# Kernel optimization log

Measured on AMD Instinct MI355X. Metric: run time of the kernel, lower is better.

Reference implementation:

```python
import jax, jax.numpy as jnp
import numpy as np

B, H, K, L, V = 4096, 1024, 10, 64, 80  # batch, hidden, mixtures, char_len, vocab

def setup_inputs() -> dict:
    key = jax.random.key(0)
    k1, k2, k3, k4 = jax.random.split(key, 4)
    return {
        "x": jax.random.normal(k1, (B, H), dtype=jnp.float32),
        "chars": jax.random.normal(k2, (B, L, V), dtype=jnp.float32),
        "W": jax.random.normal(k3, (H, 3 * K), dtype=jnp.float32) * 0.02,
        "b": jax.random.normal(k4, (3 * K,), dtype=jnp.float32) * 0.02,
    }

def reference(x, chars, W, b):
    # Linear: [B, 3K]
    out = x @ W + b
    alpha_raw, beta_raw, kappa_raw = jnp.split(out, 3, axis=1)  # each [B, K]
    alpha = jnp.exp(alpha_raw)[:, :, None]            # [B, K, 1]
    beta = jnp.exp(beta_raw)[:, :, None]              # [B, K, 1]
    # kappa_prev is zero on first call -> kappa = exp(kappa_raw)
    kappa = jnp.exp(kappa_raw)[:, :, None]            # [B, K, 1]
    u = jnp.arange(L, dtype=jnp.float32)[None, None, :]  # [1, 1, L]
    phi = jnp.sum(alpha * jnp.exp(-beta * (kappa - u) ** 2), axis=1)  # [B, L]
    window = jnp.einsum('bl,blv->bv', phi, chars)     # [B, V]
    return window
```

## Files before the change

kernel.cpp:

```cpp
#include <hip/hip_runtime.h>
#include <math.h>

constexpr int Bn = 4096;
constexpr int Hn = 1024;
constexpr int Kn = 10;
constexpr int Ln = 64;
constexpr int Vn = 80;
constexpr int NJ = 3 * Kn;
constexpr int R  = 4;
constexpr int NT = 256;

__global__ __launch_bounds__(NT) void window_kernel(
    const float* __restrict__ x,
    const float* __restrict__ chars,
    const float* __restrict__ W,
    const float* __restrict__ bias,
    float* __restrict__ out)
{
    __shared__ float  xs[R * Hn];
    __shared__ float  part[R * 256];
    __shared__ float  abk[R * NJ];
    __shared__ float  phi_s[R * Ln];
    __shared__ float4 cpart[R * 12 * 20];

    const int t    = threadIdx.x;
    const int row0 = blockIdx.x * R;

    const float4* x4  = (const float4*)x;
    float4*       xs4 = (float4*)xs;
#pragma unroll
    for (int r = 0; r < R; ++r)
        xs4[r * (Hn / 4) + t] = x4[(size_t)(row0 + r) * (Hn / 4) + t];
    __syncthreads();

    const int j = t & 31;
    const int g = t >> 5;
    float acc0 = 0.f, acc1 = 0.f, acc2 = 0.f, acc3 = 0.f;
    if (j < NJ) {
        const float* Wp = W + j;
        const int h0 = g * 128;
#pragma unroll 4
        for (int ii = 0; ii < 128; ii += 4) {
            const int h  = h0 + ii;
            const int h4 = h >> 2;
            float4 xa = xs4[0 * (Hn / 4) + h4];
            float4 xb = xs4[1 * (Hn / 4) + h4];
            float4 xc = xs4[2 * (Hn / 4) + h4];
            float4 xd = xs4[3 * (Hn / 4) + h4];
            float w0 = Wp[(h + 0) * NJ];
            float w1 = Wp[(h + 1) * NJ];
            float w2 = Wp[(h + 2) * NJ];
            float w3 = Wp[(h + 3) * NJ];
            acc0 += w0 * xa.x + w1 * xa.y + w2 * xa.z + w3 * xa.w;
            acc1 += w0 * xb.x + w1 * xb.y + w2 * xb.z + w3 * xb.w;
            acc2 += w0 * xc.x + w1 * xc.y + w2 * xc.z + w3 * xc.w;
            acc3 += w0 * xd.x + w1 * xd.y + w2 * xd.z + w3 * xd.w;
        }
    }
    part[0 * 256 + g * 32 + j] = acc0;
    part[1 * 256 + g * 32 + j] = acc1;
    part[2 * 256 + g * 32 + j] = acc2;
    part[3 * 256 + g * 32 + j] = acc3;
    __syncthreads();

    if (t < R * NJ) {
        const int r = t / NJ, jj = t % NJ;
        float s = bias[jj];
#pragma unroll
        for (int gg = 0; gg < 8; ++gg) s += part[r * 256 + gg * 32 + jj];
        abk[r * NJ + jj] = __expf(s);
    }
    __syncthreads();

    {
        const int r = t >> 6, l = t & 63;
        const float lf = (float)l;
        const float* ab = abk + r * NJ;
        float ph = 0.f;
#pragma unroll
        for (int k = 0; k < Kn; ++k) {
            float a  = ab[k];
            float bt = ab[Kn + k];
            float kp = ab[2 * Kn + k];
            float d  = kp - lf;
            ph += a * __expf(-bt * d * d);
        }
        phi_s[r * Ln + l] = ph;
    }
    __syncthreads();

    const float4* c4 = (const float4*)chars;
    if (t < 240) {
        const int v4  = t % 20;
        const int g12 = t / 20;
        float4 s0 = make_float4(0.f, 0.f, 0.f, 0.f);
        float4 s1 = s0, s2 = s0, s3 = s0;
        for (int l = g12; l < Ln; l += 12) {
            const int off = l * 20 + v4;
            float4 cA = c4[(size_t)(row0 + 0) * 1280 + off];
            float4 cB = c4[(size_t)(row0 + 1) * 1280 + off];
            float4 cC = c4[(size_t)(row0 + 2) * 1280 + off];
            float4 cD = c4[(size_t)(row0 + 3) * 1280 + off];
            float p0 = phi_s[0 * Ln + l];
            float p1 = phi_s[1 * Ln + l];
            float p2 = phi_s[2 * Ln + l];
            float p3 = phi_s[3 * Ln + l];
            s0.x += p0 * cA.x; s0.y += p0 * cA.y; s0.z += p0 * cA.z; s0.w += p0 * cA.w;
            s1.x += p1 * cB.x; s1.y += p1 * cB.y; s1.z += p1 * cB.z; s1.w += p1 * cB.w;
            s2.x += p2 * cC.x; s2.y += p2 * cC.y; s2.z += p2 * cC.z; s2.w += p2 * cC.w;
            s3.x += p3 * cD.x; s3.y += p3 * cD.y; s3.z += p3 * cD.z; s3.w += p3 * cD.w;
        }
        cpart[(0 * 12 + g12) * 20 + v4] = s0;
        cpart[(1 * 12 + g12) * 20 + v4] = s1;
        cpart[(2 * 12 + g12) * 20 + v4] = s2;
        cpart[(3 * 12 + g12) * 20 + v4] = s3;
    }
    __syncthreads();

    if (t < 80) {
        const int r  = t / 20;
        const int vv = t % 20;
        float4 s = make_float4(0.f, 0.f, 0.f, 0.f);
#pragma unroll
        for (int gg = 0; gg < 12; ++gg) {
            float4 p = cpart[(r * 12 + gg) * 20 + vv];
            s.x += p.x; s.y += p.y; s.z += p.z; s.w += p.w;
        }
        ((float4*)out)[(size_t)(row0 + r) * 20 + vv] = s;
    }
}

extern "C" void kernel_launch(void* const* d_in, const int* in_sizes, int n_in,
                              void* d_out, int out_size, void* d_ws, size_t ws_size,
                              hipStream_t stream) {
    const float* x     = (const float*)d_in[0];
    const float* chars = (const float*)d_in[1];
    const float* W     = (const float*)d_in[2];
    const float* bias  = (const float*)d_in[3];
    float* out = (float*)d_out;

    window_kernel<<<Bn / R, NT, 0, stream>>>(x, chars, W, bias, out);
}
```

Baseline: 141.7 us.

## Split fused kernel into phi kernel and lighter-weight einsum kernel via workspace

Splits the single fused kernel into two. The first computes the linear projection and phi and writes phi to the workspace buffer. The second streams chars for 2 rows per block with small shared memory, so more blocks can be resident while the bandwidth-heavy einsum runs. The fused kernel stays as a fallback when no workspace is available. This adds a second launch and a global round-trip for phi.

```diff
diff --git a/kernel.cpp b/kernel.cpp
--- a/kernel.cpp
+++ b/kernel.cpp
@@ -9,19 +9,17 @@
 constexpr int NJ = 3 * Kn;
 constexpr int R  = 4;
 constexpr int NT = 256;
-
-__global__ __launch_bounds__(NT) void window_kernel(
+constexpr int RW = 2;
+
+__global__ __launch_bounds__(NT) void phi_kernel(
     const float* __restrict__ x,
-    const float* __restrict__ chars,
     const float* __restrict__ W,
     const float* __restrict__ bias,
-    float* __restrict__ out)
+    float* __restrict__ phi)
 {
-    __shared__ float  xs[R * Hn];
-    __shared__ float  part[R * 256];
-    __shared__ float  abk[R * NJ];
-    __shared__ float  phi_s[R * Ln];
-    __shared__ float4 cpart[R * 12 * 20];
+    __shared__ float xs[R * Hn];
+    __shared__ float part[R * 256];
+    __shared__ float abk[R * NJ];
 
     const int t    = threadIdx.x;
     const int row0 = blockIdx.x * R;
@@ -85,6 +83,133 @@
             float d  = kp - lf;
             ph += a * __expf(-bt * d * d);
         }
+        phi[(size_t)(row0 + r) * Ln + l] = ph;
+    }
+}
+
+__global__ __launch_bounds__(NT) void einsum_kernel(
+    const float* __restrict__ phi,
+    const float* __restrict__ chars,
+    float* __restrict__ out)
+{
+    __shared__ float  phi_s[RW * Ln];
+    __shared__ float4 cpart[RW * 12 * 20];
+
+    const int t    = threadIdx.x;
+    const int row0 = blockIdx.x * RW;
+
+    if (t < RW * Ln)
+        phi_s[t] = phi[(size_t)row0 * Ln + t];
+    __syncthreads();
+
+    const float4* c4 = (const float4*)chars;
+    if (t < 240) {
+        const int v4 = t % 20;
+        const int g  = t / 20;
+        float4 s0 = make_float4(0.f, 0.f, 0.f, 0.f);
+        float4 s1 = s0;
+        for (int l = g; l < Ln; l += 12) {
+            const int off = l * 20 + v4;
+            float4 cA = c4[(size_t)(row0 + 0) * 1280 + off];
+            float4 cB = c4[(size_t)(row0 + 1) * 1280 + off];
+            float p0 = phi_s[l];
+            float p1 = phi_s[Ln + l];
+            s0.x += p0 * cA.x; s0.y += p0 * cA.y; s0.z += p0 * cA.z; s0.w += p0 * cA.w;
+            s1.x += p1 * cB.x; s1.y += p1 * cB.y; s1.z += p1 * cB.z; s1.w += p1 * cB.w;
+        }
+        cpart[(0 * 12 + g) * 20 + v4] = s0;
+        cpart[(1 * 12 + g) * 20 + v4] = s1;
+    }
+    __syncthreads();
+
+    if (t < RW * 20) {
+        const int r  = t / 20;
+        const int vv = t % 20;
+        float4 s = make_float4(0.f, 0.f, 0.f, 0.f);
+#pragma unroll
+        for (int gg = 0; gg < 12; ++gg) {
+            float4 p = cpart[(r * 12 + gg) * 20 + vv];
+            s.x += p.x; s.y += p.y; s.z += p.z; s.w += p.w;
+        }
+        ((float4*)out)[(size_t)(row0 + r) * 20 + vv] = s;
+    }
+}
+
+__global__ __launch_bounds__(NT) void window_kernel(
+    const float* __restrict__ x,
+    const float* __restrict__ chars,
+    const float* __restrict__ W,
+    const float* __restrict__ bias,
+    float* __restrict__ out)
+{
+    __shared__ float  xs[R * Hn];
+    __shared__ float  part[R * 256];
+    __shared__ float  abk[R * NJ];
+    __shared__ float  phi_s[R * Ln];
+    __shared__ float4 cpart[R * 12 * 20];
+
+    const int t    = threadIdx.x;
+    const int row0 = blockIdx.x * R;
+
+    const float4* x4  = (const float4*)x;
+    float4*       xs4 = (float4*)xs;
+#pragma unroll
+    for (int r = 0; r < R; ++r)
+        xs4[r * (Hn / 4) + t] = x4[(size_t)(row0 + r) * (Hn / 4) + t];
+    __syncthreads();
+
+    const int j = t & 31;
+    const int g = t >> 5;
+    float acc0 = 0.f, acc1 = 0.f, acc2 = 0.f, acc3 = 0.f;
+    if (j < NJ) {
+        const float* Wp = W + j;
+        const int h0 = g * 128;
+#pragma unroll 4
+        for (int ii = 0; ii < 128; ii += 4) {
+            const int h  = h0 + ii;
+            const int h4 = h >> 2;
+            float4 xa = xs4[0 * (Hn / 4) + h4];
+            float4 xb = xs4[1 * (Hn / 4) + h4];
+            float4 xc = xs4[2 * (Hn / 4) + h4];
+            float4 xd = xs4[3 * (Hn / 4) + h4];
+            float w0 = Wp[(h + 0) * NJ];
+            float w1 = Wp[(h + 1) * NJ];
+            float w2 = Wp[(h + 2) * NJ];
+            float w3 = Wp[(h + 3) * NJ];
+            acc0 += w0 * xa.x + w1 * xa.y + w2 * xa.z + w3 * xa.w;
+            acc1 += w0 * xb.x + w1 * xb.y + w2 * xb.z + w3 * xb.w;
+            acc2 += w0 * xc.x + w1 * xc.y + w2 * xc.z + w3 * xc.w;
+            acc3 += w0 * xd.x + w1 * xd.y + w2 * xd.z + w3 * xd.w;
+        }
+    }
+    part[0 * 256 + g * 32 + j] = acc0;
+    part[1 * 256 + g * 32 + j] = acc1;
+    part[2 * 256 + g * 32 + j] = acc2;
+    part[3 * 256 + g * 32 + j] = acc3;
+    __syncthreads();
+
+    if (t < R * NJ) {
+        const int r = t / NJ, jj = t % NJ;
+        float s = bias[jj];
+#pragma unroll
+        for (int gg = 0; gg < 8; ++gg) s += part[r * 256 + gg * 32 + jj];
+        abk[r * NJ + jj] = __expf(s);
+    }
+    __syncthreads();
+
+    {
+        const int r = t >> 6, l = t & 63;
+        const float lf = (float)l;
+        const float* ab = abk + r * NJ;
+        float ph = 0.f;
+#pragma unroll
+        for (int k = 0; k < Kn; ++k) {
+            float a  = ab[k];
+            float bt = ab[Kn + k];
+            float kp = ab[2 * Kn + k];
+            float d  = kp - lf;
+            ph += a * __expf(-bt * d * d);
+        }
         phi_s[r * Ln + l] = ph;
     }
     __syncthreads();
@@ -139,5 +264,12 @@
     const float* bias  = (const float*)d_in[3];
     float* out = (float*)d_out;
 
-    window_kernel<<<Bn / R, NT, 0, stream>>>(x, chars, W, bias, out);
-}
+    const size_t phi_bytes = (size_t)Bn * Ln * sizeof(float);
+    if (d_ws != nullptr && ws_size >= phi_bytes) {
+        float* phi = (float*)d_ws;
+        phi_kernel<<<Bn / R, NT, 0, stream>>>(x, W, bias, phi);
+        einsum_kernel<<<Bn / RW, NT, 0, stream>>>(phi, chars, out);
+    } else {
+        window_kernel<<<Bn / R, NT, 0, stream>>>(x, chars, W, bias, out);
+    }
+}
```

After: 148.7 us. 1.05x slower.

## Prefetch chars into LDS asynchronously and halve rows per block

Applied to the files above, without the earlier changes.

Issues asynchronous global-to-LDS loads of each block's chars tile at kernel start, so the memory-bound chars stream overlaps with the linear layer and phi computation. Rows per block drop from four to two, doubling the grid for more parallelism, and the sync points become raw barriers. The cost is higher LDS use, which limits occupancy, and W is reread twice as often. There is some risk of wait-count ordering issues with the async loads.

```diff
diff --git a/kernel.cpp b/kernel.cpp
--- a/kernel.cpp
+++ b/kernel.cpp
@@ -1,5 +1,6 @@
 #include <hip/hip_runtime.h>
 #include <math.h>
+#include <stdint.h>
 
 constexpr int Bn = 4096;
 constexpr int Hn = 1024;
@@ -7,35 +8,56 @@
 constexpr int Ln = 64;
 constexpr int Vn = 80;
 constexpr int NJ = 3 * Kn;
-constexpr int R  = 4;
+constexpr int R  = 2;
 constexpr int NT = 256;
 
-__global__ __launch_bounds__(NT) void window_kernel(
+typedef const __attribute__((address_space(1))) uint32_t glb_u32;
+typedef __attribute__((address_space(3))) uint32_t lds_u32;
+__device__ __forceinline__ void gload_lds16(const void* g, void* l) {
+    __builtin_amdgcn_global_load_lds((glb_u32*)g, (lds_u32*)l, 16, 0, 0);
+}
+
+__global__ __launch_bounds__(NT) void window_fused(
     const float* __restrict__ x,
     const float* __restrict__ chars,
     const float* __restrict__ W,
     const float* __restrict__ bias,
     float* __restrict__ out)
 {
-    __shared__ float  xs[R * Hn];
-    __shared__ float  part[R * 256];
+    __shared__ float4 cs4[R * Ln * Vn / 4];
+    __shared__ float4 xs4[R * Hn / 4];
+    __shared__ float  red[R * 256];
     __shared__ float  abk[R * NJ];
     __shared__ float  phi_s[R * Ln];
-    __shared__ float4 cpart[R * 12 * 20];
 
     const int t    = threadIdx.x;
+    const int lane = t & 63;
+    const int w    = t >> 6;
     const int row0 = blockIdx.x * R;
 
-    const float4* x4  = (const float4*)x;
-    float4*       xs4 = (float4*)xs;
+    const float4* xg4 = (const float4*)(x + (size_t)row0 * Hn);
+    float4 xa = xg4[t];
+    float4 xb = xg4[NT + t];
+    float bias_v = 0.f;
+    if (t < R * NJ) bias_v = bias[t % NJ];
+    xs4[t]      = xa;
+    xs4[NT + t] = xb;
+
+    const char* cg = (const char*)(chars + (size_t)row0 * Ln * Vn);
+    char*       cl = (char*)cs4;
 #pragma unroll
-    for (int r = 0; r < R; ++r)
-        xs4[r * (Hn / 4) + t] = x4[(size_t)(row0 + r) * (Hn / 4) + t];
-    __syncthreads();
+    for (int i = 0; i < 10; ++i) {
+        const int off = (w * 10 + i) * 1024;
+        gload_lds16(cg + off + lane * 16, cl + off);
+    }
+
+    asm volatile("s_waitcnt lgkmcnt(0)" ::: "memory");
+    __builtin_amdgcn_s_barrier();
+    __builtin_amdgcn_sched_barrier(0);
 
     const int j = t & 31;
     const int g = t >> 5;
-    float acc0 = 0.f, acc1 = 0.f, acc2 = 0.f, acc3 = 0.f;
+    float acc0 = 0.f, acc1 = 0.f;
     if (j < NJ) {
         const float* Wp = W + j;
         const int h0 = g * 128;
@@ -43,36 +65,34 @@
         for (int ii = 0; ii < 128; ii += 4) {
             const int h  = h0 + ii;
             const int h4 = h >> 2;
-            float4 xa = xs4[0 * (Hn / 4) + h4];
-            float4 xb = xs4[1 * (Hn / 4) + h4];
-            float4 xc = xs4[2 * (Hn / 4) + h4];
-            float4 xd = xs4[3 * (Hn / 4) + h4];
+            float4 va = xs4[h4];
+            float4 vb = xs4[(Hn / 4) + h4];
             float w0 = Wp[(h + 0) * NJ];
             float w1 = Wp[(h + 1) * NJ];
             float w2 = Wp[(h + 2) * NJ];
             float w3 = Wp[(h + 3) * NJ];
-            acc0 += w0 * xa.x + w1 * xa.y + w2 * xa.z + w3 * xa.w;
-            acc1 += w0 * xb.x + w1 * xb.y + w2 * xb.z + w3 * xb.w;
-            acc2 += w0 * xc.x + w1 * xc.y + w2 * xc.z + w3 * xc.w;
-            acc3 += w0 * xd.x + w1 * xd.y + w2 * xd.z + w3 * xd.w;
+            acc0 += w0 * va.x + w1 * va.y + w2 * va.z + w3 * va.w;
+            acc1 += w0 * vb.x + w1 * vb.y + w2 * vb.z + w3 * vb.w;
         }
     }
-    part[0 * 256 + g * 32 + j] = acc0;
-    part[1 * 256 + g * 32 + j] = acc1;
-    part[2 * 256 + g * 32 + j] = acc2;
-    part[3 * 256 + g * 32 + j] = acc3;
-    __syncthreads();
+    red[0 * 256 + g * 32 + j] = acc0;
+    red[1 * 256 + g * 32 + j] = acc1;
+    asm volatile("s_waitcnt lgkmcnt(0)" ::: "memory");
+    __builtin_amdgcn_s_barrier();
+    __builtin_amdgcn_sched_barrier(0);
 
     if (t < R * NJ) {
         const int r = t / NJ, jj = t % NJ;
-        float s = bias[jj];
+        float s = bias_v;
 #pragma unroll
-        for (int gg = 0; gg < 8; ++gg) s += part[r * 256 + gg * 32 + jj];
+        for (int gg = 0; gg < 8; ++gg) s += red[r * 256 + gg * 32 + jj];
         abk[r * NJ + jj] = __expf(s);
     }
-    __syncthreads();
+    asm volatile("s_waitcnt lgkmcnt(0)" ::: "memory");
+    __builtin_amdgcn_s_barrier();
+    __builtin_amdgcn_sched_barrier(0);
 
-    {
+    if (t < R * Ln) {
         const int r = t >> 6, l = t & 63;
         const float lf = (float)l;
         const float* ab = abk + r * NJ;
@@ -87,37 +107,29 @@
         }
         phi_s[r * Ln + l] = ph;
     }
+
     __syncthreads();
 
-    const float4* c4 = (const float4*)chars;
+    float4* cpart = (float4*)xs4;
     if (t < 240) {
         const int v4  = t % 20;
         const int g12 = t / 20;
         float4 s0 = make_float4(0.f, 0.f, 0.f, 0.f);
-        float4 s1 = s0, s2 = s0, s3 = s0;
+        float4 s1 = s0;
         for (int l = g12; l < Ln; l += 12) {
-            const int off = l * 20 + v4;
-            float4 cA = c4[(size_t)(row0 + 0) * 1280 + off];
-            float4 cB = c4[(size_t)(row0 + 1) * 1280 + off];
-            float4 cC = c4[(size_t)(row0 + 2) * 1280 + off];
-            float4 cD = c4[(size_t)(row0 + 3) * 1280 + off];
-            float p0 = phi_s[0 * Ln + l];
-            float p1 = phi_s[1 * Ln + l];
-            float p2 = phi_s[2 * Ln + l];
-            float p3 = phi_s[3 * Ln + l];
+            float4 cA = cs4[l * 20 + v4];
+            float4 cB = cs4[1280 + l * 20 + v4];
+            float p0 = phi_s[l];
+            float p1 = phi_s[Ln + l];
             s0.x += p0 * cA.x; s0.y += p0 * cA.y; s0.z += p0 * cA.z; s0.w += p0 * cA.w;
             s1.x += p1 * cB.x; s1.y += p1 * cB.y; s1.z += p1 * cB.z; s1.w += p1 * cB.w;
-            s2.x += p2 * cC.x; s2.y += p2 * cC.y; s2.z += p2 * cC.z; s2.w += p2 * cC.w;
-            s3.x += p3 * cD.x; s3.y += p3 * cD.y; s3.z += p3 * cD.z; s3.w += p3 * cD.w;
         }
         cpart[(0 * 12 + g12) * 20 + v4] = s0;
         cpart[(1 * 12 + g12) * 20 + v4] = s1;
-        cpart[(2 * 12 + g12) * 20 + v4] = s2;
-        cpart[(3 * 12 + g12) * 20 + v4] = s3;
     }
     __syncthreads();
 
-    if (t < 80) {
+    if (t < R * 20) {
         const int r  = t / 20;
         const int vv = t % 20;
         float4 s = make_float4(0.f, 0.f, 0.f, 0.f);
@@ -139,5 +151,5 @@
     const float* bias  = (const float*)d_in[3];
     float* out = (float*)d_out;
 
-    window_kernel<<<Bn / R, NT, 0, stream>>>(x, chars, W, bias, out);
+    window_fused<<<Bn / R, NT, 0, stream>>>(x, chars, W, bias, out);
 }
```

Result: slower. 148.5 us (+4.8%).

## Map one wavefront per row for window reduction and reduce via shuffles

Applied to the files above, without the earlier changes.

The chars-weighted reduction is remapped so each 64-lane wavefront handles one batch row. Lanes split into three l-strided groups of 20 float4 columns, and the partials are combined with wave shuffles instead of a shared-memory cpart buffer and an extra barrier. This removes the last __syncthreads and the serial 12-way shared reduction, and shrinks shared memory. Launch bounds now request 7 blocks per CU for occupancy. Lanes 60-63 do redundant loads, and each lane performs more serial iterations (up to 22).

```diff
diff --git a/kernel.cpp b/kernel.cpp
--- a/kernel.cpp
+++ b/kernel.cpp
@@ -10,27 +10,25 @@
 constexpr int R  = 4;
 constexpr int NT = 256;
 
-__global__ __launch_bounds__(NT) void window_kernel(
+__global__ __launch_bounds__(NT, 7) void window_fused(
     const float* __restrict__ x,
     const float* __restrict__ chars,
     const float* __restrict__ W,
     const float* __restrict__ bias,
     float* __restrict__ out)
 {
-    __shared__ float  xs[R * Hn];
+    __shared__ float4 xs4[R * Hn / 4];
     __shared__ float  part[R * 256];
     __shared__ float  abk[R * NJ];
     __shared__ float  phi_s[R * Ln];
-    __shared__ float4 cpart[R * 12 * 20];
 
     const int t    = threadIdx.x;
     const int row0 = blockIdx.x * R;
 
-    const float4* x4  = (const float4*)x;
-    float4*       xs4 = (float4*)xs;
+    const float4* xg4 = (const float4*)x + (size_t)row0 * (Hn / 4);
 #pragma unroll
     for (int r = 0; r < R; ++r)
-        xs4[r * (Hn / 4) + t] = x4[(size_t)(row0 + r) * (Hn / 4) + t];
+        xs4[r * (Hn / 4) + t] = xg4[r * (Hn / 4) + t];
     __syncthreads();
 
     const int j = t & 31;
@@ -89,45 +87,34 @@
     }
     __syncthreads();
 
-    const float4* c4 = (const float4*)chars;
-    if (t < 240) {
-        const int v4  = t % 20;
-        const int g12 = t / 20;
-        float4 s0 = make_float4(0.f, 0.f, 0.f, 0.f);
-        float4 s1 = s0, s2 = s0, s3 = s0;
-        for (int l = g12; l < Ln; l += 12) {
-            const int off = l * 20 + v4;
-            float4 cA = c4[(size_t)(row0 + 0) * 1280 + off];
-            float4 cB = c4[(size_t)(row0 + 1) * 1280 + off];
-            float4 cC = c4[(size_t)(row0 + 2) * 1280 + off];
-            float4 cD = c4[(size_t)(row0 + 3) * 1280 + off];
-            float p0 = phi_s[0 * Ln + l];
-            float p1 = phi_s[1 * Ln + l];
-            float p2 = phi_s[2 * Ln + l];
-            float p3 = phi_s[3 * Ln + l];
-            s0.x += p0 * cA.x; s0.y += p0 * cA.y; s0.z += p0 * cA.z; s0.w += p0 * cA.w;
-            s1.x += p1 * cB.x; s1.y += p1 * cB.y; s1.z += p1 * cB.z; s1.w += p1 * cB.w;
-            s2.x += p2 * cC.x; s2.y += p2 * cC.y; s2.z += p2 * cC.z; s2.w += p2 * cC.w;
-            s3.x += p3 * cD.x; s3.y += p3 * cD.y; s3.z += p3 * cD.z; s3.w += p3 * cD.w;
+    const int lane = t & 63;
+    const int rr   = t >> 6;
+    const int ll = (lane < 60) ? lane : lane - 60;
+    const int ls = ll / 20;
+    const int v4 = ll % 20;
+
+    const float4* cb = (const float4*)chars + (size_t)(row0 + rr) * (Ln * Vn / 4);
+    const float*  ph = phi_s + rr * Ln;
+
+    float4 acc = make_float4(0.f, 0.f, 0.f, 0.f);
+#pragma unroll
+    for (int i = 0; i < 22; ++i) {
+        const int l = ls + 3 * i;
+        if (l < Ln) {
+            float4 c = cb[l * (Vn / 4) + v4];
+            float  p = ph[l];
+            acc.x += p * c.x; acc.y += p * c.y;
+            acc.z += p * c.z; acc.w += p * c.w;
         }
-        cpart[(0 * 12 + g12) * 20 + v4] = s0;
-        cpart[(1 * 12 + g12) * 20 + v4] = s1;
-        cpart[(2 * 12 + g12) * 20 + v4] = s2;
-        cpart[(3 * 12 + g12) * 20 + v4] = s3;
     }
-    __syncthreads();
 
-    if (t < 80) {
-        const int r  = t / 20;
-        const int vv = t % 20;
-        float4 s = make_float4(0.f, 0.f, 0.f, 0.f);
-#pragma unroll
-        for (int gg = 0; gg < 12; ++gg) {
-            float4 p = cpart[(r * 12 + gg) * 20 + vv];
-            s.x += p.x; s.y += p.y; s.z += p.z; s.w += p.w;
-        }
-        ((float4*)out)[(size_t)(row0 + r) * 20 + vv] = s;
-    }
+    acc.x += __shfl(acc.x, lane + 20) + __shfl(acc.x, lane + 40);
+    acc.y += __shfl(acc.y, lane + 20) + __shfl(acc.y, lane + 40);
+    acc.z += __shfl(acc.z, lane + 20) + __shfl(acc.z, lane + 40);
+    acc.w += __shfl(acc.w, lane + 20) + __shfl(acc.w, lane + 40);
+
+    if (lane < 20)
+        ((float4*)out)[(size_t)(row0 + rr) * (Vn / 4) + lane] = acc;
 }
 
 extern "C" void kernel_launch(void* const* d_in, const int* in_sizes, int n_in,
@@ -139,5 +126,5 @@
     const float* bias  = (const float*)d_in[3];
     float* out = (float*)d_out;
 
-    window_kernel<<<Bn / R, NT, 0, stream>>>(x, chars, W, bias, out);
+    window_fused<<<Bn / R, NT, 0, stream>>>(x, chars, W, bias, out);
 }
```

Result: slower. 152.7 us (+7.8%).
